# Kernel optimization log

Measured on AMD Instinct MI355X. Metric: run time of the kernel, lower is better.

The kernel has to match this reference:

```python
import jax, jax.numpy as jnp
import numpy as np

BATCH = 8192
INPUT_DIM = 10240
NODES = 1024          # == INPUT_DIM // 10, required by compressed @ adjacency
ACTIONS = 64
HIDDEN = 128
BINS = 100
HLO, HHI = -5.0, 5.0
ENTROPY_THRESH = 2.5


def _semantic_mask(n):
    m = np.zeros((n, n), dtype=np.float32)
    m[9, 0] = 1.0; m[9, 1] = 1.0; m[3, 0] = 1.0; m[2, 7] = 1.0; m[6, 4] = 1.0
    np.fill_diagonal(m, 1.0)
    m[8, 5] = 1.0; m[8, 1] = 1.0; m[8, 3] = 1.0
    if n > 6:
        m[5, 6] = 10.0
        m[1, 6] = 5.0
    if n > 5:
        m[5, 3] = 2.0
    return jnp.asarray(m)


def setup_inputs() -> dict:
    key = jax.random.key(0)
    ks = jax.random.split(key, 6)
    event_stream = jax.random.normal(ks[0], (BATCH, INPUT_DIM), dtype=jnp.float32)
    sensing_matrix = jax.random.normal(ks[1], (INPUT_DIM // 10, INPUT_DIM), dtype=jnp.float32)
    # adjacency is a trainable parameter (zeros at init); use small random values
    # so the downstream state/policy computation is non-degenerate.
    adjacency = 0.01 * jax.random.normal(ks[2], (NODES, NODES), dtype=jnp.float32)
    semantic_mask = _semantic_mask(NODES)
    W1 = jax.random.normal(ks[3], (HIDDEN, NODES), dtype=jnp.float32) / np.sqrt(NODES)
    b1 = jnp.zeros((HIDDEN,), dtype=jnp.float32)
    W2 = jax.random.normal(ks[4], (ACTIONS, HIDDEN), dtype=jnp.float32) / np.sqrt(HIDDEN)
    b2 = jnp.zeros((ACTIONS,), dtype=jnp.float32)
    return {"event_stream": event_stream, "sensing_matrix": sensing_matrix,
            "adjacency": adjacency, "semantic_mask": semantic_mask,
            "W1": W1, "b1": b1, "W2": W2, "b2": b2}


def _batched_histc(x):
    # Faithful vectorized torch.histc(bins=100, min=-5, max=5):
    # out-of-range values are ignored; values == max land in the last bin.
    b = x.shape[0]
    idx = jnp.clip(jnp.floor((x - HLO) / (HHI - HLO) * BINS).astype(jnp.int32), 0, BINS - 1)
    in_range = ((x >= HLO) & (x <= HHI)).astype(x.dtype)
    rows = jnp.broadcast_to(jnp.arange(b)[:, None], x.shape)
    return jnp.zeros((b, BINS), dtype=x.dtype).at[rows, idx].add(in_range)


def _policy(s, W1, b1, W2, b2):
    h = jax.nn.relu(s @ W1.T + b1)
    return h @ W2.T + b2


def reference(event_stream, sensing_matrix, adjacency, semantic_mask, W1, b1, W2, b2):
    # --- Layer 1: information filter (batched histogram + Shannon entropy gate) ---
    hist = _batched_histc(event_stream)                       # [B, 100]
    prob = hist / (hist.sum(-1, keepdims=True) + 1e-9)
    h_ent = -(prob * jnp.log(prob + 1e-9)).sum(-1)            # [B]
    compressed = event_stream @ sensing_matrix.T              # [B, NODES]
    keep = (h_ent >= ENTROPY_THRESH)[:, None].astype(compressed.dtype)
    filtered = compressed * keep                              # zeros where low entropy

    # --- Layer 2: causal forward ---
    state = filtered @ adjacency                              # [B, NODES]

    # --- Semantic consistency loss ---
    semantic_loss = jnp.sum(jnp.abs(adjacency) * semantic_mask)

    # --- Layer 3: robust Nash policy (training path: sign-grad perturbation) ---
    grad_s = jax.grad(lambda s: _policy(s, W1, b1, W2, b2).mean())(state)
    perturbation = jnp.sign(grad_s)
    robust_logits = _policy(state - 0.1 * perturbation, W1, b1, W2, b2)
    action_probs = jax.nn.softmax(robust_logits, axis=-1)     # [B, ACTIONS]

    return action_probs, adjacency, semantic_loss
```

## Files before the change

### kernel.cpp

```cpp
#include <hip/hip_runtime.h>
#include <hip/hip_bf16.h>

typedef unsigned short u16;
typedef short v8s __attribute__((ext_vector_type(8)));
typedef float v4f __attribute__((ext_vector_type(4)));

#define BATCH 8192
#define IND 10240
#define NODES 1024
#define ACTIONS 64
#define HIDDEN 128

__device__ __forceinline__ u16 f2b(float x) {
    __hip_bfloat16 h = __float2bfloat16(x);
    return *reinterpret_cast<u16*>(&h);
}

__device__ __forceinline__ float b2f(u16 x) {
    unsigned u = ((unsigned)x) << 16;
    return *reinterpret_cast<float*>(&u);
}

__device__ __forceinline__ void gload16(const void* g, void* l) {
    __builtin_amdgcn_global_load_lds(
        (const __attribute__((address_space(1))) void*)g,
        (__attribute__((address_space(3))) void*)l, 16, 0, 0);
}

__global__ __launch_bounds__(256) void hist_entropy_cast(
    const float* __restrict__ E, u16* __restrict__ Ebf, float* __restrict__ keep)
{
    __shared__ int hist[4][100];
    const int tid = threadIdx.x;
    const int wave = tid >> 6;
    const int b = blockIdx.x;
    for (int j = tid; j < 400; j += 256) ((int*)hist)[j] = 0;
    __syncthreads();

    const float* row = E + (size_t)b * IND;
    u16* orow = Ebf + (size_t)b * IND;
    for (int i = tid * 4; i < IND; i += 1024) {
        float4 v = *reinterpret_cast<const float4*>(row + i);
        float xs[4] = {v.x, v.y, v.z, v.w};
        u16 ob[4];
#pragma unroll
        for (int j = 0; j < 4; ++j) {
            float x = xs[j];
            ob[j] = f2b(x);
            if (x >= -5.0f && x <= 5.0f) {
                int idx = (int)floorf((x + 5.0f) / 10.0f * 100.0f);
                idx = idx < 0 ? 0 : (idx > 99 ? 99 : idx);
                atomicAdd(&hist[wave][idx], 1);
            }
        }
        u16 packed[4] = {ob[0], ob[1], ob[2], ob[3]};
        *reinterpret_cast<uint2*>(orow + i) = *reinterpret_cast<uint2*>(packed);
    }
    __syncthreads();
    if (tid < 100)
        hist[0][tid] = hist[0][tid] + hist[1][tid] + hist[2][tid] + hist[3][tid];
    __syncthreads();

    if (tid < 64) {
        float c0 = (float)hist[0][tid];
        float c1 = (tid < 36) ? (float)hist[0][tid + 64] : 0.0f;
        float tot = c0 + c1;
#pragma unroll
        for (int s = 32; s >= 1; s >>= 1) tot += __shfl_xor(tot, s);
        float denom = tot + 1e-9f;
        float p0 = c0 / denom, p1 = c1 / denom;
        float e = -(p0 * logf(p0 + 1e-9f)) - (p1 * logf(p1 + 1e-9f));
#pragma unroll
        for (int s = 32; s >= 1; s >>= 1) e += __shfl_xor(e, s);
        if (tid == 0) keep[b] = (e >= 2.5f) ? 1.0f : 0.0f;
    }
}

__global__ __launch_bounds__(256) void cvt_bf16(
    const float* __restrict__ in, u16* __restrict__ out, long n4)
{
    long i = (long)blockIdx.x * blockDim.x + threadIdx.x;
    const long stride = (long)gridDim.x * blockDim.x;
    for (; i < n4; i += stride) {
        float4 v = reinterpret_cast<const float4*>(in)[i];
        u16 o[4] = {f2b(v.x), f2b(v.y), f2b(v.z), f2b(v.w)};
        reinterpret_cast<uint2*>(out)[i] = *reinterpret_cast<uint2*>(o);
    }
}

__global__ void transpose_cvt(const float* __restrict__ in, u16* __restrict__ out,
                              int R, int C)
{
    __shared__ float t[32][33];
    const int bx = blockIdx.x * 32, by = blockIdx.y * 32;
    const int tx = threadIdx.x, ty = threadIdx.y;
#pragma unroll
    for (int j = 0; j < 32; j += 8) {
        int r = by + ty + j, c = bx + tx;
        if (r < R && c < C) t[ty + j][tx] = in[(size_t)r * C + c];
    }
    __syncthreads();
#pragma unroll
    for (int j = 0; j < 32; j += 8) {
        int oc = by + tx;
        int orow = bx + ty + j;
        if (orow < C && oc < R) out[(size_t)orow * R + oc] = f2b(t[tx][ty + j]);
    }
}

__global__ void w2sum_k(const float* __restrict__ W2, float* __restrict__ w2s)
{
    int i = threadIdx.x;
    if (i < HIDDEN) {
        float s = 0.f;
        for (int a = 0; a < ACTIONS; ++a) s += W2[a * HIDDEN + i];
        w2s[i] = s;
    }
}

__global__ __launch_bounds__(256) void semloss1(
    const float* __restrict__ A, const float* __restrict__ M, float* __restrict__ part)
{
    const int tid = threadIdx.x;
    float s = 0.f;
    for (int i = blockIdx.x * 256 + tid; i < NODES * NODES; i += 256 * gridDim.x)
        s += fabsf(A[i]) * M[i];
    __shared__ float ws[4];
#pragma unroll
    for (int off = 32; off >= 1; off >>= 1) s += __shfl_xor(s, off);
    if ((tid & 63) == 0) ws[tid >> 6] = s;
    __syncthreads();
    if (tid == 0) part[blockIdx.x] = ws[0] + ws[1] + ws[2] + ws[3];
}

__global__ void semloss2(const float* __restrict__ part, float* __restrict__ out, int n)
{
    const int tid = threadIdx.x;
    float s = (tid < n) ? part[tid] : 0.f;
    __shared__ float ws[4];
#pragma unroll
    for (int off = 32; off >= 1; off >>= 1) s += __shfl_xor(s, off);
    if ((tid & 63) == 0) ws[tid >> 6] = s;
    __syncthreads();
    if (tid == 0) out[0] = ws[0] + ws[1] + ws[2] + ws[3];
}

template<int EP>
__global__ __launch_bounds__(256) void gemm_bt(
    const u16* __restrict__ A, const u16* __restrict__ B, int K, int N,
    const float* __restrict__ aux0, const float* __restrict__ aux1,
    u16* __restrict__ outb)
{
    __shared__ u16 As[2][128 * 64];
    __shared__ u16 Bs[2][128 * 64];
    const int tid = threadIdx.x;
    const int wave = tid >> 6, lane = tid & 63;
    const int wr = wave >> 1, wc = wave & 1;
    const int l15 = lane & 15, lhi = lane >> 4;
    const int swz = (l15 & 7) << 3;
    const int src_c = (((lane & 7) ^ (lane >> 3)) << 3);
    const int src_r = lane >> 3;
    const u16* Ag = A + (size_t)(blockIdx.x * 128) * K;
    const u16* Bg = B + (size_t)(blockIdx.y * 128) * K;

    v4f acc[4][4];
#pragma unroll
    for (int m = 0; m < 4; ++m)
#pragma unroll
        for (int n = 0; n < 4; ++n) acc[m][n] = (v4f){0.f, 0.f, 0.f, 0.f};

#pragma unroll
    for (int i = 0; i < 4; ++i) {
        int chunk = wave * 4 + i;
        int r = chunk * 8 + src_r;
        gload16(Ag + (size_t)r * K + src_c, &As[0][chunk * 512]);
        gload16(Bg + (size_t)r * K + src_c, &Bs[0][chunk * 512]);
    }
    __syncthreads();

    int cur = 0;
    for (int kt = 0; kt < K; kt += 64) {
        if (kt + 64 < K) {
            int nxt = cur ^ 1;
#pragma unroll
            for (int i = 0; i < 4; ++i) {
                int chunk = wave * 4 + i;
                int r = chunk * 8 + src_r;
                gload16(Ag + (size_t)r * K + (kt + 64 + src_c), &As[nxt][chunk * 512]);
                gload16(Bg + (size_t)r * K + (kt + 64 + src_c), &Bs[nxt][chunk * 512]);
            }
        }
#pragma unroll
        for (int ks = 0; ks < 2; ++ks) {
            v8s a[4], b[4];
#pragma unroll
            for (int m = 0; m < 4; ++m)
                a[m] = *reinterpret_cast<const v8s*>(
                    &As[cur][(wr * 64 + m * 16 + l15) * 64 + ((ks * 32 + (lhi << 3)) ^ swz)]);
#pragma unroll
            for (int n = 0; n < 4; ++n)
                b[n] = *reinterpret_cast<const v8s*>(
                    &Bs[cur][(wc * 64 + n * 16 + l15) * 64 + ((ks * 32 + (lhi << 3)) ^ swz)]);
#pragma unroll
            for (int m = 0; m < 4; ++m)
#pragma unroll
                for (int n = 0; n < 4; ++n)
                    acc[m][n] = __builtin_amdgcn_mfma_f32_16x16x32_bf16(
                        a[m], b[n], acc[m][n], 0, 0, 0);
        }
        __syncthreads();
        cur ^= 1;
    }

    const int m0 = blockIdx.x * 128 + wr * 64;
    const int n0 = blockIdx.y * 128 + wc * 64;
#pragma unroll
    for (int m = 0; m < 4; ++m) {
#pragma unroll
        for (int j = 0; j < 4; ++j) {
            int row = m0 + m * 16 + (lhi << 2) + j;
#pragma unroll
            for (int n = 0; n < 4; ++n) {
                int col = n0 + n * 16 + l15;
                float v = acc[m][n][j];
                size_t off = (size_t)row * N + col;
                if (EP == 0) {
                    outb[off] = f2b(v * aux0[row]);
                } else if (EP == 1) {
                    outb[off] = f2b(v);
                } else if (EP == 2) {
                    float h = v + aux0[col];
                    outb[off] = (h > 0.f) ? f2b(aux1[col]) : (u16)0;
                } else {
                    float sg = (v > 0.f) ? 1.f : ((v < 0.f) ? -1.f : 0.f);
                    float sv = b2f(((const u16*)aux0)[off]);
                    outb[off] = f2b(sv - 0.1f * sg);
                }
            }
        }
    }
}

__global__ __launch_bounds__(256) void policy_final(
    const u16* __restrict__ S2, const u16* __restrict__ W1b,
    const float* __restrict__ b1, const u16* __restrict__ W2b,
    const float* __restrict__ b2, float* __restrict__ probs)
{
    __shared__ u16 As[128 * 64];
    __shared__ u16 Bs[128 * 64];
    __shared__ u16 H2[128 * 128];
    const int tid = threadIdx.x;
    const int wave = tid >> 6, lane = tid & 63;
    const int wr = wave >> 1, wc = wave & 1;
    const int l15 = lane & 15, lhi = lane >> 4;
    const int swz = (l15 & 7) << 3;
    const int src_c = (((lane & 7) ^ (lane >> 3)) << 3);
    const int src_r = lane >> 3;
    const u16* Ag = S2 + (size_t)(blockIdx.x * 128) * NODES;

    v4f acc[4][4];
#pragma unroll
    for (int m = 0; m < 4; ++m)
#pragma unroll
        for (int n = 0; n < 4; ++n) acc[m][n] = (v4f){0.f, 0.f, 0.f, 0.f};

    for (int kt = 0; kt < NODES; kt += 64) {
#pragma unroll
        for (int i = 0; i < 4; ++i) {
            int chunk = wave * 4 + i;
            int r = chunk * 8 + src_r;
            gload16(Ag + (size_t)r * NODES + (kt + src_c), &As[chunk * 512]);
            gload16(W1b + (size_t)r * NODES + (kt + src_c), &Bs[chunk * 512]);
        }
        __syncthreads();
#pragma unroll
        for (int ks = 0; ks < 2; ++ks) {
            v8s a[4], b[4];
#pragma unroll
            for (int m = 0; m < 4; ++m)
                a[m] = *reinterpret_cast<const v8s*>(
                    &As[(wr * 64 + m * 16 + l15) * 64 + ((ks * 32 + (lhi << 3)) ^ swz)]);
#pragma unroll
            for (int n = 0; n < 4; ++n)
                b[n] = *reinterpret_cast<const v8s*>(
                    &Bs[(wc * 64 + n * 16 + l15) * 64 + ((ks * 32 + (lhi << 3)) ^ swz)]);
#pragma unroll
            for (int m = 0; m < 4; ++m)
#pragma unroll
                for (int n = 0; n < 4; ++n)
                    acc[m][n] = __builtin_amdgcn_mfma_f32_16x16x32_bf16(
                        a[m], b[n], acc[m][n], 0, 0, 0);
        }
        __syncthreads();
    }

#pragma unroll
    for (int m = 0; m < 4; ++m)
#pragma unroll
        for (int j = 0; j < 4; ++j) {
            int lrow = wr * 64 + m * 16 + (lhi << 2) + j;
#pragma unroll
            for (int n = 0; n < 4; ++n) {
                int col = wc * 64 + n * 16 + l15;
                float v = acc[m][n][j] + b1[col];
                H2[lrow * 128 + (col ^ ((lrow & 7) << 3))] = f2b(v > 0.f ? v : 0.f);
            }
        }
#pragma unroll
    for (int i = 0; i < 4; ++i) {
        int e = (tid + i * 256) * 8;
        int row = e >> 7, col = e & 127;
        int dst = (row << 7) | (col ^ ((row & 7) << 3));
        *reinterpret_cast<v8s*>(&Bs[dst]) = *reinterpret_cast<const v8s*>(&W2b[e]);
    }
    __syncthreads();

    v4f a2[2][4];
#pragma unroll
    for (int m = 0; m < 2; ++m)
#pragma unroll
        for (int n = 0; n < 4; ++n) a2[m][n] = (v4f){0.f, 0.f, 0.f, 0.f};
#pragma unroll
    for (int ks = 0; ks < 4; ++ks) {
        v8s af[2], bf[4];
#pragma unroll
        for (int m = 0; m < 2; ++m)
            af[m] = *reinterpret_cast<const v8s*>(
                &H2[(wave * 32 + m * 16 + l15) * 128 + ((ks * 32 + (lhi << 3)) ^ swz)]);
#pragma unroll
        for (int n = 0; n < 4; ++n)
            bf[n] = *reinterpret_cast<const v8s*>(
                &Bs[(n * 16 + l15) * 128 + ((ks * 32 + (lhi << 3)) ^ swz)]);
#pragma unroll
        for (int m = 0; m < 2; ++m)
#pragma unroll
            for (int n = 0; n < 4; ++n)
                a2[m][n] = __builtin_amdgcn_mfma_f32_16x16x32_bf16(
                    af[m], bf[n], a2[m][n], 0, 0, 0);
    }

#pragma unroll
    for (int m = 0; m < 2; ++m) {
#pragma unroll
        for (int j = 0; j < 4; ++j) {
            int lrow = wave * 32 + m * 16 + (lhi << 2) + j;
            float v[4];
#pragma unroll
            for (int n = 0; n < 4; ++n) v[n] = a2[m][n][j] + b2[n * 16 + l15];
            float mx = fmaxf(fmaxf(v[0], v[1]), fmaxf(v[2], v[3]));
#pragma unroll
            for (int s = 8; s >= 1; s >>= 1) mx = fmaxf(mx, __shfl_xor(mx, s));
            float e[4], sum = 0.f;
#pragma unroll
            for (int n = 0; n < 4; ++n) { e[n] = expf(v[n] - mx); sum += e[n]; }
#pragma unroll
            for (int s = 8; s >= 1; s >>= 1) sum += __shfl_xor(sum, s);
            float inv = 1.0f / sum;
            size_t base = (size_t)(blockIdx.x * 128 + lrow) * ACTIONS;
#pragma unroll
            for (int n = 0; n < 4; ++n) probs[base + n * 16 + l15] = e[n] * inv;
        }
    }
}

extern "C" void kernel_launch(void* const* d_in, const int* in_sizes, int n_in,
                              void* d_out, int out_size, void* d_ws, size_t ws_size,
                              hipStream_t stream)
{
    const float* E   = (const float*)d_in[0];
    const float* S   = (const float*)d_in[1];
    const float* Adj = (const float*)d_in[2];
    const float* Msk = (const float*)d_in[3];
    const float* W1  = (const float*)d_in[4];
    const float* b1  = (const float*)d_in[5];
    const float* W2  = (const float*)d_in[6];
    const float* b2  = (const float*)d_in[7];
    float* out = (float*)d_out;

    char* ws = (char*)d_ws;
    u16*  Ebf  = (u16*)  (ws + 0UL);
    u16*  Sbf  = (u16*)  (ws + 167772160UL);
    u16*  Atb  = (u16*)  (ws + 188743680UL);
    u16*  W1b  = (u16*)  (ws + 190840832UL);
    u16*  W1tb = (u16*)  (ws + 191102976UL);
    u16*  W2b  = (u16*)  (ws + 191365120UL);
    float* w2s = (float*)(ws + 191381504UL);
    float* keep= (float*)(ws + 191382016UL);
    float* part= (float*)(ws + 191414784UL);
    u16*  filt = (u16*)  (ws + 191415808UL);
    u16*  stb  = (u16*)  (ws + 208193024UL);
    u16*  dbuf = (u16*)  (ws + 224970240UL);
    u16*  s2   = (u16*)  (ws + 227067392UL);

    dim3 tb(32, 8);
    hist_entropy_cast<<<8192, 256, 0, stream>>>(E, Ebf, keep);
    cvt_bf16<<<2048, 256, 0, stream>>>(S, Sbf, (long)NODES * IND / 4);
    cvt_bf16<<<128, 256, 0, stream>>>(W1, W1b, (long)HIDDEN * NODES / 4);
    cvt_bf16<<<8, 256, 0, stream>>>(W2, W2b, (long)ACTIONS * HIDDEN / 4);
    transpose_cvt<<<dim3(32, 32), tb, 0, stream>>>(Adj, Atb, NODES, NODES);
    transpose_cvt<<<dim3(32, 4),  tb, 0, stream>>>(W1, W1tb, HIDDEN, NODES);
    w2sum_k<<<1, 128, 0, stream>>>(W2, w2s);
    semloss1<<<256, 256, 0, stream>>>(Adj, Msk, part);
    semloss2<<<1, 256, 0, stream>>>(part, out + 524288 + 1048576, 256);
    hipMemcpyAsync(out + 524288, Adj, sizeof(float) * 1048576,
                   hipMemcpyDeviceToDevice, stream);

    gemm_bt<0><<<dim3(64, 8), 256, 0, stream>>>(Ebf, Sbf, IND, NODES,
                                                keep, nullptr, filt);
    gemm_bt<1><<<dim3(64, 8), 256, 0, stream>>>(filt, Atb, NODES, NODES,
                                                nullptr, nullptr, stb);
    gemm_bt<2><<<dim3(64, 1), 256, 0, stream>>>(stb, W1b, NODES, HIDDEN,
                                                b1, w2s, dbuf);
    gemm_bt<3><<<dim3(64, 8), 256, 0, stream>>>(dbuf, W1tb, HIDDEN, NODES,
                                                (const float*)stb, nullptr, s2);
    policy_final<<<64, 256, 0, stream>>>(s2, W1b, b1, W2b, b2, out);
}
```

Before: 432.9 us.

## Replace compression GEMM with 256x256 split-K pipelined MFMA kernel plus combine pass

Replaces the 128x128-tile event_stream x sensing_matrix GEMM with a new 512-thread kernel. It uses 256x256 output tiles, a two-way split over K, and 128KB of dynamic LDS with double-buffered global-to-LDS loads. MFMA phases are interleaved with staging through explicit barriers, vmcnt waits and setprio. The split-K fp32 partials are then summed, scaled by the entropy keep mask and cast to bf16 in a separate combine kernel. This raises reuse per tile and MFMA density, at the cost of writing and re-reading about 64MB of fp32 partials; that buffer reuses workspace later taken by stb, dbuf and s2.

```diff
diff --git a/kernel.cpp b/kernel.cpp
--- a/kernel.cpp
+++ b/kernel.cpp
@@ -26,6 +26,11 @@
         (const __attribute__((address_space(1))) void*)g,
         (__attribute__((address_space(3))) void*)l, 16, 0, 0);
 }
+
+#define SBAR() do { __builtin_amdgcn_s_barrier(); \
+                    __builtin_amdgcn_sched_barrier(0); } while (0)
+#define VMCNT4() asm volatile("s_waitcnt vmcnt(4)" ::: "memory")
+#define VMCNT0() asm volatile("s_waitcnt vmcnt(0)" ::: "memory")
 
 __global__ __launch_bounds__(256) void hist_entropy_cast(
     const float* __restrict__ E, u16* __restrict__ Ebf, float* __restrict__ keep)
@@ -143,6 +148,136 @@
     if ((tid & 63) == 0) ws[tid >> 6] = s;
     __syncthreads();
     if (tid == 0) out[0] = ws[0] + ws[1] + ws[2] + ws[3];
+}
+
+__global__ __launch_bounds__(256) void combine_keep(
+    const float* __restrict__ p0, const float* __restrict__ p1,
+    const float* __restrict__ keep, u16* __restrict__ filt)
+{
+    long base = ((long)blockIdx.x * 256 + threadIdx.x) * 4;
+    float4 a = *reinterpret_cast<const float4*>(p0 + base);
+    float4 b = *reinterpret_cast<const float4*>(p1 + base);
+    float k = keep[base >> 10];
+    u16 o[4] = {f2b((a.x + b.x) * k), f2b((a.y + b.y) * k),
+                f2b((a.z + b.z) * k), f2b((a.w + b.w) * k)};
+    *reinterpret_cast<uint2*>(filt + base) = *reinterpret_cast<uint2*>(o);
+}
+
+__device__ __forceinline__ void stage_chunk(
+    const u16* __restrict__ g, char* lds, int chunk_off, int kt_col,
+    int tid, int wave)
+{
+    const int s_row0 = tid >> 2;
+    const int gblk = (tid & 3) ^ ((tid >> 3) & 3);
+#pragma unroll
+    for (int j = 0; j < 2; ++j) {
+        int lrow = j * 128 + s_row0;
+        gload16(g + (size_t)lrow * IND + kt_col + (gblk << 3),
+                lds + chunk_off + j * 8192 + (wave << 10));
+    }
+}
+
+__global__ __launch_bounds__(512, 2) void gemm8_ep0(
+    const u16* __restrict__ A, const u16* __restrict__ B,
+    float* __restrict__ outf)
+{
+    extern __shared__ char lds[];
+    const int tid = threadIdx.x;
+    const int wave = tid >> 6, lane = tid & 63;
+    const int wr = wave >> 2, wcn = wave & 3;
+    const int l15 = lane & 15, lhi = lane >> 4;
+    const int rsw = (lhi ^ ((l15 >> 1) & 3)) << 4;
+    const size_t koff = (size_t)blockIdx.z * (IND / 2);
+    const u16* Ag = A + (size_t)(blockIdx.x * 256) * IND + koff;
+    const u16* Bg = B + (size_t)(blockIdx.y * 256) * IND + koff;
+
+    v4f acc[8][4];
+#pragma unroll
+    for (int m = 0; m < 8; ++m)
+#pragma unroll
+        for (int n = 0; n < 4; ++n) acc[m][n] = (v4f){0.f, 0.f, 0.f, 0.f};
+
+    v8s a[8], b0, b1;
+    const int arow = wr * 128 * 64;
+    const int brow0 = wcn * 64 * 64;
+
+#define LDA(P, KS, M) (*reinterpret_cast<const v8s*>( \
+    lds + ((P)*2 + (KS)) * 16384 + arow + ((M)*16 + l15) * 64 + rsw))
+#define LDB(P, KS, NF) (*reinterpret_cast<const v8s*>( \
+    lds + 65536 + ((P)*2 + (KS)) * 16384 + brow0 + ((NF)*16 + l15) * 64 + rsw))
+#define MFMA2(NH) do { \
+    _Pragma("unroll") \
+    for (int m = 0; m < 8; ++m) { \
+        acc[m][2*(NH)]   = __builtin_amdgcn_mfma_f32_16x16x32_bf16( \
+            a[m], b0, acc[m][2*(NH)], 0, 0, 0); \
+        acc[m][2*(NH)+1] = __builtin_amdgcn_mfma_f32_16x16x32_bf16( \
+            a[m], b1, acc[m][2*(NH)+1], 0, 0, 0); \
+    } } while (0)
+
+#define TILE(P, KTN, STG) do { \
+     \
+    _Pragma("unroll") \
+    for (int m = 0; m < 8; ++m) a[m] = LDA(P, 0, m); \
+    b0 = LDB(P, 0, 0); b1 = LDB(P, 0, 1); \
+    if (STG) stage_chunk(Ag, lds, ((P^1)*2 + 0) * 16384, (KTN), tid, wave); \
+    SBAR(); \
+    __builtin_amdgcn_s_setprio(1); MFMA2(0); __builtin_amdgcn_s_setprio(0); \
+    SBAR(); \
+     \
+    b0 = LDB(P, 0, 2); b1 = LDB(P, 0, 3); \
+    if (STG) { stage_chunk(Bg, lds, 65536 + ((P^1)*2 + 0) * 16384, (KTN), tid, wave); \
+               VMCNT4(); } else { VMCNT0(); } \
+    SBAR(); \
+    __builtin_amdgcn_s_setprio(1); MFMA2(1); __builtin_amdgcn_s_setprio(0); \
+    SBAR(); \
+     \
+    _Pragma("unroll") \
+    for (int m = 0; m < 8; ++m) a[m] = LDA(P, 1, m); \
+    b0 = LDB(P, 1, 0); b1 = LDB(P, 1, 1); \
+    if (STG) stage_chunk(Ag, lds, ((P^1)*2 + 1) * 16384, (KTN) + 32, tid, wave); \
+    SBAR(); \
+    __builtin_amdgcn_s_setprio(1); MFMA2(0); __builtin_amdgcn_s_setprio(0); \
+    SBAR(); \
+     \
+    b0 = LDB(P, 1, 2); b1 = LDB(P, 1, 3); \
+    if (STG) { stage_chunk(Bg, lds, 65536 + ((P^1)*2 + 1) * 16384, (KTN) + 32, tid, wave); \
+               VMCNT4(); } \
+    SBAR(); \
+    __builtin_amdgcn_s_setprio(1); MFMA2(1); __builtin_amdgcn_s_setprio(0); \
+    SBAR(); \
+} while (0)
+
+    stage_chunk(Ag, lds, 0 * 16384, 0, tid, wave);
+    stage_chunk(Bg, lds, 65536 + 0 * 16384, 0, tid, wave);
+    stage_chunk(Ag, lds, 1 * 16384, 32, tid, wave);
+    stage_chunk(Bg, lds, 65536 + 1 * 16384, 32, tid, wave);
+    VMCNT4();
+    SBAR();
+
+#pragma unroll 1
+    for (int tp = 0; tp < 39; ++tp) {
+        TILE(0, (2 * tp + 1) * 64, 1);
+        TILE(1, (2 * tp + 2) * 64, 1);
+    }
+    TILE(0, 79 * 64, 1);
+    TILE(1, 0, 0);
+
+#undef TILE
+#undef MFMA2
+#undef LDB
+#undef LDA
+
+    const size_t zo = (size_t)blockIdx.z * ((size_t)BATCH * NODES);
+    const int grow0 = blockIdx.x * 256 + wr * 128 + (lhi << 2);
+    const int gcol0 = blockIdx.y * 256 + wcn * 64 + l15;
+#pragma unroll
+    for (int m = 0; m < 8; ++m)
+#pragma unroll
+        for (int n = 0; n < 4; ++n)
+#pragma unroll
+            for (int j = 0; j < 4; ++j)
+                outf[zo + (size_t)(grow0 + m * 16 + j) * NODES + gcol0 + n * 16] =
+                    acc[m][n][j];
 }
 
 template<int EP>
@@ -224,9 +359,7 @@
                 int col = n0 + n * 16 + l15;
                 float v = acc[m][n][j];
                 size_t off = (size_t)row * N + col;
-                if (EP == 0) {
-                    outb[off] = f2b(v * aux0[row]);
-                } else if (EP == 1) {
+                if (EP == 1) {
                     outb[off] = f2b(v);
                 } else if (EP == 2) {
                     float h = v + aux0[col];
@@ -388,9 +521,13 @@
     float* keep= (float*)(ws + 191382016UL);
     float* part= (float*)(ws + 191414784UL);
     u16*  filt = (u16*)  (ws + 191415808UL);
+    float* pbuf = (float*)(ws + 208193024UL);
     u16*  stb  = (u16*)  (ws + 208193024UL);
     u16*  dbuf = (u16*)  (ws + 224970240UL);
     u16*  s2   = (u16*)  (ws + 227067392UL);
+
+    hipFuncSetAttribute((const void*)gemm8_ep0,
+                        hipFuncAttributeMaxDynamicSharedMemorySize, 131072);
 
     dim3 tb(32, 8);
     hist_entropy_cast<<<8192, 256, 0, stream>>>(E, Ebf, keep);
@@ -405,8 +542,9 @@
     hipMemcpyAsync(out + 524288, Adj, sizeof(float) * 1048576,
                    hipMemcpyDeviceToDevice, stream);
 
-    gemm_bt<0><<<dim3(64, 8), 256, 0, stream>>>(Ebf, Sbf, IND, NODES,
-                                                keep, nullptr, filt);
+    gemm8_ep0<<<dim3(32, 4, 2), 512, 131072, stream>>>(Ebf, Sbf, pbuf);
+    combine_keep<<<8192, 256, 0, stream>>>(pbuf, pbuf + (size_t)BATCH * NODES,
+                                           keep, filt);
     gemm_bt<1><<<dim3(64, 8), 256, 0, stream>>>(filt, Atb, NODES, NODES,
                                                 nullptr, nullptr, stb);
     gemm_bt<2><<<dim3(64, 1), 256, 0, stream>>>(stb, W1b, NODES, HIDDEN,
```

Result: faster. 388.1 us (-10.3%).

## Replace main compression GEMM with 8-wave 256x128 pipelined MFMA kernel

Applied to the files above, without the earlier changes.

The large E×Sᵀ GEMM (K=10240) moves from the generic 128x128 4-wave kernel to a dedicated 512-thread kernel with 256x128 tiles. It uses a four-stage LDS buffer of 32-wide K slices, explicit vmcnt waits and barriers so global-to-LDS loads overlap MFMA work, an XOR swizzle, and s_setprio around the MFMA bursts. The goal is better data reuse and latency hiding in the dominant GEMM. In exchange it needs 96 KB of dynamic LDS, hand-tuned waitcnt ordering that is fragile, and a grid of only 256 blocks.

```diff
diff --git a/kernel.cpp b/kernel.cpp
--- a/kernel.cpp
+++ b/kernel.cpp
@@ -26,6 +26,11 @@
         (const __attribute__((address_space(1))) void*)g,
         (__attribute__((address_space(3))) void*)l, 16, 0, 0);
 }
+
+#define SBAR() do { __builtin_amdgcn_s_barrier(); \
+                    __builtin_amdgcn_sched_barrier(0); } while (0)
+#define VMCNT3() asm volatile("s_waitcnt vmcnt(3)" ::: "memory")
+#define VMCNT0() asm volatile("s_waitcnt vmcnt(0)" ::: "memory")
 
 __global__ __launch_bounds__(256) void hist_entropy_cast(
     const float* __restrict__ E, u16* __restrict__ Ebf, float* __restrict__ keep)
@@ -143,6 +148,106 @@
     if ((tid & 63) == 0) ws[tid >> 6] = s;
     __syncthreads();
     if (tid == 0) out[0] = ws[0] + ws[1] + ws[2] + ws[3];
+}
+
+template<int NJ>
+__device__ __forceinline__ void stage_rows(
+    const u16* __restrict__ g, char* lds_base, int kt_col, int tid, int wave)
+{
+    const int s_row0 = tid >> 2;
+    const int gblk = (tid & 3) ^ ((tid >> 3) & 3);
+#pragma unroll
+    for (int j = 0; j < NJ; ++j)
+        gload16(g + (size_t)(j * 128 + s_row0) * IND + kt_col + (gblk << 3),
+                lds_base + j * 8192 + (wave << 10));
+}
+
+__global__ __launch_bounds__(512, 2) void gemm8_keep(
+    const u16* __restrict__ A, const u16* __restrict__ B,
+    const float* __restrict__ keep, u16* __restrict__ outb)
+{
+    extern __shared__ char lds[];
+    const int tid = threadIdx.x;
+    const int wave = tid >> 6, lane = tid & 63;
+    const int wr = wave >> 2, wcn = wave & 3;
+    const int l15 = lane & 15, lhi = lane >> 4;
+    const int rsw = (lhi ^ ((l15 >> 1) & 3)) << 4;
+    const u16* Ag = A + (size_t)(blockIdx.x * 256) * IND;
+    const u16* Bg = B + (size_t)(blockIdx.y * 128) * IND;
+
+    v4f acc[8][2];
+#pragma unroll
+    for (int m = 0; m < 8; ++m) {
+        acc[m][0] = (v4f){0.f, 0.f, 0.f, 0.f};
+        acc[m][1] = (v4f){0.f, 0.f, 0.f, 0.f};
+    }
+
+    v8s a[8], b0, b1;
+    const int arow = wr * 128 * 64;
+    const int brow = wcn * 32 * 64;
+
+#define LDA(P, KS, M) (*reinterpret_cast<const v8s*>( \
+    lds + ((P)*2 + (KS)) * 16384 + arow + ((M)*16 + l15) * 64 + rsw))
+#define LDB(P, KS, NF) (*reinterpret_cast<const v8s*>( \
+    lds + 65536 + ((P)*2 + (KS)) * 8192 + brow + ((NF)*16 + l15) * 64 + rsw))
+
+#define PHASE(P, KS, KTN, STG, DRAIN) do { \
+    _Pragma("unroll") \
+    for (int m = 0; m < 8; ++m) a[m] = LDA(P, KS, m); \
+    b0 = LDB(P, KS, 0); b1 = LDB(P, KS, 1); \
+    if (STG) { \
+        stage_rows<2>(Ag, lds + (((P)^1)*2 + (KS)) * 16384, \
+                      (KTN) + (KS)*32, tid, wave); \
+        stage_rows<1>(Bg, lds + 65536 + (((P)^1)*2 + (KS)) * 8192, \
+                      (KTN) + (KS)*32, tid, wave); \
+        VMCNT3(); \
+    } else if (DRAIN) { VMCNT0(); } \
+    SBAR(); \
+    __builtin_amdgcn_s_setprio(1); \
+    _Pragma("unroll") \
+    for (int m = 0; m < 8; ++m) { \
+        acc[m][0] = __builtin_amdgcn_mfma_f32_16x16x32_bf16(a[m], b0, acc[m][0], 0, 0, 0); \
+        acc[m][1] = __builtin_amdgcn_mfma_f32_16x16x32_bf16(a[m], b1, acc[m][1], 0, 0, 0); \
+    } \
+    __builtin_amdgcn_s_setprio(0); \
+    SBAR(); \
+} while (0)
+
+#define TILE(P, KTN)  do { PHASE(P, 0, KTN, 1, 0); PHASE(P, 1, KTN, 1, 0); } while (0)
+
+    stage_rows<2>(Ag, lds + 0 * 16384, 0, tid, wave);
+    stage_rows<1>(Bg, lds + 65536 + 0 * 8192, 0, tid, wave);
+    stage_rows<2>(Ag, lds + 1 * 16384, 32, tid, wave);
+    stage_rows<1>(Bg, lds + 65536 + 1 * 8192, 32, tid, wave);
+    VMCNT3();
+    SBAR();
+
+#pragma unroll 1
+    for (int tp = 0; tp < 79; ++tp) {
+        TILE(0, (2 * tp + 1) * 64);
+        TILE(1, (2 * tp + 2) * 64);
+    }
+    TILE(0, 159 * 64);
+    PHASE(1, 0, 0, 0, 1);
+    PHASE(1, 1, 0, 0, 0);
+
+#undef TILE
+#undef PHASE
+#undef LDB
+#undef LDA
+
+    const int grow0 = blockIdx.x * 256 + wr * 128 + (lhi << 2);
+    const int gcol0 = blockIdx.y * 128 + wcn * 32 + l15;
+#pragma unroll
+    for (int m = 0; m < 8; ++m) {
+#pragma unroll
+        for (int j = 0; j < 4; ++j) {
+            int row = grow0 + m * 16 + j;
+            float k = keep[row];
+            outb[(size_t)row * NODES + gcol0]      = f2b(acc[m][0][j] * k);
+            outb[(size_t)row * NODES + gcol0 + 16] = f2b(acc[m][1][j] * k);
+        }
+    }
 }
 
 template<int EP>
@@ -224,9 +329,7 @@
                 int col = n0 + n * 16 + l15;
                 float v = acc[m][n][j];
                 size_t off = (size_t)row * N + col;
-                if (EP == 0) {
-                    outb[off] = f2b(v * aux0[row]);
-                } else if (EP == 1) {
+                if (EP == 1) {
                     outb[off] = f2b(v);
                 } else if (EP == 2) {
                     float h = v + aux0[col];
@@ -392,6 +495,9 @@
     u16*  dbuf = (u16*)  (ws + 224970240UL);
     u16*  s2   = (u16*)  (ws + 227067392UL);
 
+    hipFuncSetAttribute((const void*)gemm8_keep,
+                        hipFuncAttributeMaxDynamicSharedMemorySize, 98304);
+
     dim3 tb(32, 8);
     hist_entropy_cast<<<8192, 256, 0, stream>>>(E, Ebf, keep);
     cvt_bf16<<<2048, 256, 0, stream>>>(S, Sbf, (long)NODES * IND / 4);
@@ -405,8 +511,7 @@
     hipMemcpyAsync(out + 524288, Adj, sizeof(float) * 1048576,
                    hipMemcpyDeviceToDevice, stream);
 
-    gemm_bt<0><<<dim3(64, 8), 256, 0, stream>>>(Ebf, Sbf, IND, NODES,
-                                                keep, nullptr, filt);
+    gemm8_keep<<<dim3(32, 8), 512, 98304, stream>>>(Ebf, Sbf, keep, filt);
     gemm_bt<1><<<dim3(64, 8), 256, 0, stream>>>(filt, Atb, NODES, NODES,
                                                 nullptr, nullptr, stb);
     gemm_bt<2><<<dim3(64, 1), 256, 0, stream>>>(stb, W1b, NODES, HIDDEN,
```

Result: slower. 455.6 us (+5.3%).
